# Kernel tuning notes

Hardware: AMD Instinct MI355X
Metric: run time of the kernel (lower is better)

## Reference

```python
import jax, jax.numpy as jnp
import numpy as np

NUM_CLASSES = 41
EPS = 1e-12


def nearest_resize(lab, h, w):
    # torch F.interpolate(mode='nearest'): src_idx = floor(dst_idx * in / out)
    Hl, Wl = lab.shape[1], lab.shape[2]
    ih = (jnp.arange(h) * Hl) // h
    iw = (jnp.arange(w) * Wl) // w
    return lab[:, ih][:, :, iw]


def segment_mean(feats, lab_small, base):
    # feats [b,c,h,w], lab_small [b,h,w] int, base [b,L,c] (values for absent labels)
    b, c, h, w = feats.shape
    L = NUM_CLASSES
    lab = lab_small.reshape(b, h * w)
    ids = (jnp.arange(b, dtype=lab.dtype)[:, None] * L + lab).reshape(-1)  # [b*h*w]
    x = feats.reshape(b, c, h * w).transpose(0, 2, 1).reshape(-1, c)       # [b*h*w, c]
    sums = jax.ops.segment_sum(x, ids, num_segments=b * L).reshape(b, L, c)
    cnts = jax.ops.segment_sum(jnp.ones((b * h * w,), feats.dtype), ids,
                               num_segments=b * L).reshape(b, L, 1)
    mean = sums / jnp.maximum(cnts, 1.0)
    return jnp.where(cnts > 0, mean, base)


def ra_gate(feats, lab_small, base, w1, w2):
    # RA.forward: segment-mean queue -> L2 normalize over class dim -> sum -> 1x1 convs -> sigmoid
    att = segment_mean(feats, lab_small, base)                      # [b,L,c]
    nrm = jnp.sqrt(jnp.sum(att * att, axis=1, keepdims=True))       # over classes (dim=1)
    att = att / jnp.maximum(nrm, EPS)
    s = jnp.sum(att, axis=1)                                        # [b,c]
    h1 = jax.nn.relu(jnp.einsum('bc,oc->bo', s, w1))                # conv1 1x1, no bias
    g = jax.nn.sigmoid(jnp.einsum('bo,co->bc', h1, w2))             # conv2 1x1, no bias
    return g[:, :, None, None]                                      # [b,c,1,1]


def conv3x3(x, w):
    return jax.lax.conv_general_dilated(
        x, w, window_strides=(1, 1), padding=((1, 1), (1, 1)),
        dimension_numbers=('NCHW', 'OIHW', 'NCHW'))


def setup_inputs() -> dict:
    key = jax.random.key(0)
    ks = jax.random.split(key, 10)
    B, C, H, W = 8, 128, 128, 128
    return {
        'r': jax.random.normal(ks[0], (B, C, H, W), jnp.float32),
        'd': jax.random.normal(ks[1], (B, C, H, W), jnp.float32),
        'label': jax.random.randint(ks[2], (B, 4 * H, 4 * W), 0, NUM_CLASSES, jnp.int32),
        'conv_w': jax.random.normal(ks[3], (C, 2 * C, 3, 3), jnp.float32) * 0.05,
        'f_w1': jax.random.normal(ks[4], (C // 16, C), jnp.float32) * 0.05,
        'f_w2': jax.random.normal(ks[5], (C, C // 16), jnp.float32) * 0.05,
        'd_w1': jax.random.normal(ks[6], (C // 16, C), jnp.float32) * 0.05,
        'd_w2': jax.random.normal(ks[7], (C, C // 16), jnp.float32) * 0.05,
        'seg_base_f': jax.random.normal(ks[8], (B, NUM_CLASSES, C), jnp.float32),
        'seg_base_d': jax.random.normal(ks[9], (B, NUM_CLASSES, C), jnp.float32),
    }


def reference(r, d, label, conv_w, f_w1, f_w2, d_w1, d_w2, seg_base_f, seg_base_d):
    b, c, h, w = r.shape
    add = r + d
    mul = r * jax.nn.sigmoid(d)
    fuse = conv3x3(jnp.concatenate([add, mul], axis=1), conv_w)
    lab_small = nearest_resize(label, h, w)
    d_ra = d * ra_gate(d, lab_small, seg_base_d, d_w1, d_w2)
    fuse_ra = fuse * ra_gate(fuse, lab_small, seg_base_f, f_w1, f_w2)
    return fuse_ra + d_ra
```

## Files before the change

kernel.cpp:

```cpp
#include <hip/hip_runtime.h>
#include <math.h>

typedef unsigned short u16;
typedef unsigned char u8;
typedef unsigned int u32;
typedef unsigned long long u64;
typedef __bf16 bf16x8 __attribute__((ext_vector_type(8)));
typedef float f32x4 __attribute__((ext_vector_type(4)));

#define NL 41
#define HW 16384

#define NHWC_OFF   0
#define WA_OFF     67108864
#define LAB8_OFF   67698688
#define SUMS_OFF   67829760
#define GATES_OFF  68165632
#define PD_OFF     68173824
#define PD_END     78921728ull

#define PSZ 5248

__device__ __forceinline__ u16 f2bf(float f) {
    u32 u = __builtin_bit_cast(u32, f);
    u = (u + 0x7FFFu + ((u >> 16) & 1u)) >> 16;
    return (u16)u;
}

__device__ __forceinline__ void glds16(const void* g, void* l) {
    __builtin_amdgcn_global_load_lds(
        (const __attribute__((address_space(1))) void*)g,
        (__attribute__((address_space(3))) void*)l, 16, 0, 0);
}

__global__ __launch_bounds__(256, 2)
void k_prep(const float* __restrict__ r, const float* __restrict__ d,
            const int* __restrict__ label, const float* __restrict__ w,
            u16* __restrict__ nhwc, u16* __restrict__ wa,
            u8* __restrict__ lab8, float* __restrict__ pd)
{
    __shared__ u16 s[64 * 256];
    __shared__ float binsd[NL * 256];
    __shared__ u8 s_lab[256];
    const int bid = (int)blockIdx.x;
    const int b = bid >> 6;
    const int px0 = (bid & 63) * 256;
    const int tid = (int)threadIdx.x;
    const int c = tid & 127;
    const int half = tid >> 7;

    if (bid < 144) {
        const int wi = bid * 4 + (tid >> 6);
        const int l = tid & 63;
        const int kt = wi >> 3, ct = wi & 7;
        const int chunk = kt / 9, tap = kt - chunk * 9;
        const int co = ct * 16 + (l & 15);
        const int cin0 = chunk * 32 + (l >> 4) * 8;
        u16 tmp[8];
#pragma unroll
        for (int j = 0; j < 8; ++j)
            tmp[j] = f2bf(w[((size_t)co * 256 + cin0 + j) * 9 + tap]);
        *(f32x4*)&wa[((size_t)wi * 64 + l) * 8] = *(f32x4*)tmp;
    }

    for (int i = tid; i < NL * 64; i += 256) ((f32x4*)binsd)[i] = f32x4{0,0,0,0};

    {
        int px = px0 + tid;
        int yy = px >> 7, xx = px & 127;
        int lab = label[(size_t)b * 512 * 512 + (yy * 4) * 512 + xx * 4];
        lab8[b * HW + px] = (u8)lab;
        s_lab[tid] = (u8)lab;
    }
    __syncthreads();

    for (int t = 0; t < 4; ++t) {
        const int pxb = px0 + t * 64 + half * 32;
        const float* rp = r + ((size_t)(b * 128 + c)) * HW + pxb;
        const float* dp = d + ((size_t)(b * 128 + c)) * HW + pxb;
        const u8* lp = &s_lab[t * 64 + half * 32];
        uint4 lw0 = *(const uint4*)lp;
        uint4 lw1 = *(const uint4*)(lp + 16);
        u32 lwords[8] = {lw0.x, lw0.y, lw0.z, lw0.w, lw1.x, lw1.y, lw1.z, lw1.w};
#pragma unroll
        for (int j = 0; j < 8; ++j) {
            float4 rv = *(const float4*)(rp + j * 4);
            float4 dv = *(const float4*)(dp + j * 4);
            float ra[4] = {rv.x, rv.y, rv.z, rv.w};
            float da[4] = {dv.x, dv.y, dv.z, dv.w};
#pragma unroll
            for (int i = 0; i < 4; ++i) {
                int pxl = half * 32 + j * 4 + i;
                s[pxl * 256 + c] = f2bf(ra[i] + da[i]);
                s[pxl * 256 + 128 + c] = f2bf(ra[i] / (1.f + __expf(-da[i])));
                int lab = (int)((lwords[j] >> (i * 8)) & 0xffu);
                binsd[lab * 256 + tid] += da[i];
            }
        }
        __syncthreads();
        const f32x4* sf = (const f32x4*)s;
        f32x4* dst = (f32x4*)nhwc + ((size_t)b * HW + px0 + t * 64) * 32;
#pragma unroll
        for (int k = 0; k < 8; ++k) {
            int fi = k * 256 + tid;
            dst[fi] = sf[fi];
        }
        __syncthreads();
    }
    float* pout = pd + (size_t)bid * PSZ;
    for (int i = tid; i < NL * 128; i += 256) {
        int lab = i >> 7, cc = i & 127;
        pout[i] = binsd[lab * 256 + cc] + binsd[lab * 256 + 128 + cc];
    }
}

__global__ __launch_bounds__(256, 2)
void k_conv(const u16* __restrict__ nhwc, const u16* __restrict__ wa,
            float* __restrict__ out)
{
    __shared__ u16 s_in[2 * 2080 * 8];
    const int tid = (int)threadIdx.x;
    const int bid = (int)blockIdx.x;
    const int b = bid & 7;
    const int y0 = (bid >> 3) * 2;
    const int l = tid & 63;
    const int wv = tid >> 6;
    const int wr = wv & 1;
    const int wc = wv >> 1;
    const int l15 = l & 15;
    const int l16 = l >> 4;

    {
        f32x4 zz = {0.f, 0.f, 0.f, 0.f};
        for (int i = tid; i < 4160; i += 256) ((f32x4*)s_in)[i] = zz;
    }

    int goff[9];
#pragma unroll
    for (int it = 0; it < 9; ++it) {
        int s = it * 256 + tid;
        int row = s / 520;
        int rem = s - row * 520;
        int xslot = rem >> 2;
        int ci8 = rem & 3;
        int gy = y0 - 1 + row;
        int gx = xslot - 1;
        bool valid = (s < 2080) && ((unsigned)gy < 128u) && ((unsigned)gx < 128u);
        goff[it] = valid ? (((gy << 7) | gx) * 256 + ci8 * 8) * 2 : -1;
    }

    f32x4 acc[4][8];
#pragma unroll
    for (int i = 0; i < 4; ++i)
#pragma unroll
        for (int j = 0; j < 8; ++j) {
            f32x4 zz = {0.f, 0.f, 0.f, 0.f};
            acc[i][j] = zz;
        }

    const char* src_b = (const char*)(nhwc + (size_t)b * HW * 256);
    const int lane_base = (tid & 192) * 16;
    const f32x4* wa4 = (const f32x4*)wa;

    __syncthreads();
#pragma unroll
    for (int it = 0; it < 9; ++it)
        if (goff[it] >= 0)
            glds16(src_b + goff[it], (char*)s_in + it * 4096 + lane_base);

#pragma unroll 1
    for (int chunk = 0; chunk < 8; ++chunk) {
        __syncthreads();

        f32x4 a0[4], a1[4];
        {
            int kt8 = chunk * 72;
#pragma unroll
            for (int i = 0; i < 4; ++i) a0[i] = wa4[(kt8 + wc * 4 + i) * 64 + l];
#pragma unroll
            for (int i = 0; i < 4; ++i) a1[i] = wa4[(kt8 + 8 + wc * 4 + i) * 64 + l];
        }
        if (chunk < 7) {
            char* dstb = (char*)s_in + ((chunk + 1) & 1) * 33280 + lane_base;
#pragma unroll
            for (int it = 0; it < 9; ++it)
                if (goff[it] >= 0)
                    glds16(src_b + goff[it] + (chunk + 1) * 64, dstb + it * 4096);
        }

        const char* bufp = (const char*)s_in + (chunk & 1) * 33280;
#pragma unroll
        for (int tap = 0; tap < 9; ++tap) {
            f32x4 aC[4];
#pragma unroll
            for (int i = 0; i < 4; ++i) aC[i] = a0[i];
#pragma unroll
            for (int i = 0; i < 4; ++i) a0[i] = a1[i];
            if (tap + 2 < 9) {
                int kt8 = chunk * 72 + (tap + 2) * 8;
#pragma unroll
                for (int i = 0; i < 4; ++i)
                    a1[i] = wa4[(kt8 + wc * 4 + i) * 64 + l];
            }
            const int rowi = wr + tap / 3;
            const int dxo = tap % 3;
            f32x4 bf[8];
#pragma unroll
            for (int p = 0; p < 8; ++p) {
                int e = (rowi * 130 + p * 16 + l15 + dxo) * 64 + l16 * 16;
                bf[p] = *(const f32x4*)(bufp + e);
            }
#pragma unroll
            for (int ct = 0; ct < 4; ++ct) {
                bf16x8 av = __builtin_bit_cast(bf16x8, aC[ct]);
#pragma unroll
                for (int p = 0; p < 8; ++p)
                    acc[ct][p] = __builtin_amdgcn_mfma_f32_16x16x32_bf16(
                        av, __builtin_bit_cast(bf16x8, bf[p]), acc[ct][p], 0, 0, 0);
            }
        }
    }

    const int y = y0 + wr;
    float* outb = out + (size_t)b * 128 * HW + (size_t)y * 128;
#pragma unroll
    for (int ct = 0; ct < 4; ++ct)
#pragma unroll
        for (int p = 0; p < 8; ++p) {
            int x = p * 16 + l15;
#pragma unroll
            for (int rr = 0; rr < 4; ++rr) {
                int co = wc * 64 + ct * 16 + l16 * 4 + rr;
                outb[(size_t)co * HW + x] = acc[ct][p][rr];
            }
        }
}

__global__ __launch_bounds__(256, 3)
void k_seg2(const float* __restrict__ fuse, const float* __restrict__ pd,
            const u8* __restrict__ lab8, float* __restrict__ sums_f,
            float* __restrict__ sums_d)
{
    __shared__ float bins[NL][256];
    const int bid = (int)blockIdx.x;
    const int tid = (int)threadIdx.x;

    if (bid >= 1024) {
        const int idx = bid - 1024;
        if (tid < 128) {
            const int b = idx / 41, lab = idx - b * 41;
            const float* q = pd + (size_t)b * 64 * PSZ + lab * 128 + tid;
            float sv = 0.f;
#pragma unroll 8
            for (int k = 0; k < 64; ++k) sv += q[(size_t)k * PSZ];
            sums_d[(size_t)idx * 128 + tid] = sv;
        }
        return;
    }

    const int c = bid & 127;
    const int b = bid >> 7;

    for (int i = tid; i < NL * 256; i += 256) ((float*)bins)[i] = 0.f;
    __syncthreads();

    const float* src = fuse + ((size_t)(b * 128 + c)) * HW;
    const u8* lp = lab8 + b * HW;

#pragma unroll 4
    for (int k = 0; k < 16; ++k) {
        int i = k * 256 + tid;
        float4 v = ((const float4*)src)[i];
        uchar4 lv = ((const uchar4*)lp)[i];
        bins[lv.x][tid] += v.x;
        bins[lv.y][tid] += v.y;
        bins[lv.z][tid] += v.z;
        bins[lv.w][tid] += v.w;
    }
    __syncthreads();

    for (int stride = 128; stride >= 1; stride >>= 1) {
        for (int idx = tid; idx < NL * stride; idx += 256) {
            int l = idx / stride;
            int cc = idx - l * stride;
            bins[l][cc] += bins[l][cc + stride];
        }
        __syncthreads();
    }
    if (tid < NL)
        sums_f[(size_t)(b * NL + tid) * 128 + c] = bins[tid][0];
}

__global__ __launch_bounds__(128)
void k_gates(const float* __restrict__ sums, const u8* __restrict__ lab8,
             const float* __restrict__ base_f, const float* __restrict__ base_d,
             const float* __restrict__ f_w1, const float* __restrict__ f_w2,
             const float* __restrict__ d_w1, const float* __restrict__ d_w2,
             float* __restrict__ gates)
{
    __shared__ float sv[128];
    __shared__ float h1[8];
    __shared__ int hist[NL];
    const int b = (int)blockIdx.x >> 1;
    const int feat = (int)blockIdx.x & 1;
    const int c = (int)threadIdx.x;

    if (c < NL) hist[c] = 0;
    __syncthreads();
    {
        const uchar4* lp = (const uchar4*)(lab8 + (size_t)b * HW);
        for (int k = 0; k < 32; ++k) {
            uchar4 lv = lp[c + k * 128];
            atomicAdd(&hist[lv.x], 1);
            atomicAdd(&hist[lv.y], 1);
            atomicAdd(&hist[lv.z], 1);
            atomicAdd(&hist[lv.w], 1);
        }
    }
    __syncthreads();

    const float* base = feat ? base_d : base_f;
    const float* sf = sums + (size_t)feat * 8 * NL * 128;
    float suma = 0.f, sumsq = 0.f;
    for (int lc = 0; lc < NL; ++lc) {
        float s = sf[(size_t)(b * NL + lc) * 128 + c];
        int cnt = hist[lc];
        float att = (cnt > 0) ? (s / (float)cnt) : base[(b * NL + lc) * 128 + c];
        suma += att;
        sumsq += att * att;
    }
    sv[c] = suma / fmaxf(sqrtf(sumsq), 1e-12f);
    __syncthreads();

    const float* w1 = feat ? d_w1 : f_w1;
    const float* w2 = feat ? d_w2 : f_w2;
    if (c < 8) {
        float h = 0.f;
        for (int k = 0; k < 128; ++k) h += w1[c * 128 + k] * sv[k];
        h1[c] = fmaxf(h, 0.f);
    }
    __syncthreads();

    float gv = 0.f;
#pragma unroll
    for (int o = 0; o < 8; ++o) gv += w2[c * 8 + o] * h1[o];
    gates[feat * 1024 + b * 128 + c] = 1.f / (1.f + expf(-gv));
}

__global__ __launch_bounds__(256)
void k_final(const float* __restrict__ d, const float* __restrict__ gates,
             float* out)
{
    const size_t base = (size_t)blockIdx.x * 256 + threadIdx.x;
#pragma unroll
    for (int it = 0; it < 8; ++it) {
        size_t t4 = base + (size_t)it * (2048 * 256);
        size_t basei = t4 * 4;
        int bc = (int)(basei >> 14);
        float gf = gates[bc];
        float gd = gates[1024 + bc];
        float4 f = *(const float4*)(out + basei);
        float4 dv = *(const float4*)(d + basei);
        float4 o;
        o.x = f.x * gf + dv.x * gd;
        o.y = f.y * gf + dv.y * gd;
        o.z = f.z * gf + dv.z * gd;
        o.w = f.w * gf + dv.w * gd;
        *(float4*)(out + basei) = o;
    }
}

__global__ __launch_bounds__(128)
void k_red(const float* __restrict__ p, float* __restrict__ sout)
{
    const int bid = (int)blockIdx.x;
    const int b = bid / 41, lab = bid - b * 41;
    const int c = (int)threadIdx.x;
    const float* q = p + (size_t)b * 64 * PSZ + lab * 128 + c;
    float s = 0.f;
#pragma unroll 8
    for (int k = 0; k < 64; ++k) s += q[(size_t)k * PSZ];
    sout[(size_t)bid * 128 + c] = s;
}

extern "C" void kernel_launch(void* const* d_in, const int* in_sizes, int n_in,
                              void* d_out, int out_size, void* d_ws, size_t ws_size,
                              hipStream_t stream)
{
    (void)in_sizes; (void)n_in; (void)out_size;
    const float* r      = (const float*)d_in[0];
    const float* d      = (const float*)d_in[1];
    const int*   label  = (const int*)d_in[2];
    const float* conv_w = (const float*)d_in[3];
    const float* f_w1   = (const float*)d_in[4];
    const float* f_w2   = (const float*)d_in[5];
    const float* d_w1   = (const float*)d_in[6];
    const float* d_w2   = (const float*)d_in[7];
    const float* base_f = (const float*)d_in[8];
    const float* base_d = (const float*)d_in[9];
    float* out = (float*)d_out;

    char* ws = (char*)d_ws;
    u16* nhwc     = (u16*)(ws + NHWC_OFF);
    u16* wa       = (u16*)(ws + WA_OFF);
    u8*  lab8     = (u8*)(ws + LAB8_OFF);
    float* sums   = (float*)(ws + SUMS_OFF);
    float* sums_f = sums;
    float* sums_d = sums + 8 * NL * 128;
    float* gates  = (float*)(ws + GATES_OFF);

    const bool big = ws_size >= PD_END;
    float* pd = big ? (float*)(ws + PD_OFF) : (float*)d_out;

    hipLaunchKernelGGL(k_prep, dim3(512), dim3(256), 0, stream, r, d, label,
                       conv_w, nhwc, wa, lab8, pd);
    if (!big)
        hipLaunchKernelGGL(k_red, dim3(328), dim3(128), 0, stream, pd, sums_d);
    hipLaunchKernelGGL(k_conv, dim3(512), dim3(256), 0, stream, nhwc, wa, out);
    hipLaunchKernelGGL(k_seg2, dim3(big ? 1352 : 1024), dim3(256), 0, stream,
                       out, pd, lab8, sums_f, sums_d);
    hipLaunchKernelGGL(k_gates, dim3(16), dim3(128), 0, stream, sums, lab8,
                       base_f, base_d, f_w1, f_w2, d_w1, d_w2, gates);
    hipLaunchKernelGGL(k_final, dim3(2048), dim3(256), 0, stream, d, gates, out);
}
```

Measured before the change: 368.5 us.

## Split conv tiles along width and move label histogram into prep kernel

The conv kernel now tiles 2 rows by 64 columns instead of 2 full rows. This halves LDS use and accumulator registers, doubles the grid to 1024 blocks and raises the launch-bounds occupancy hint to 3. The cost is extra halo reloads at the column split. Per-batch label counts are now built inside k_prep with shared atomics and merged into a global histogram, which is zeroed by a memset first. This takes the serial 16-block histogram loop out of k_gates, at the price of an extra memset and global atomics.

```diff
diff --git a/kernel.cpp b/kernel.cpp
--- a/kernel.cpp
+++ b/kernel.cpp
@@ -16,8 +16,9 @@
 #define LAB8_OFF   67698688
 #define SUMS_OFF   67829760
 #define GATES_OFF  68165632
-#define PD_OFF     68173824
-#define PD_END     78921728ull
+#define GH_OFF     68173824
+#define PD_OFF     68177920
+#define PD_END     78925824ull
 
 #define PSZ 5248
 
@@ -37,11 +38,13 @@
 void k_prep(const float* __restrict__ r, const float* __restrict__ d,
             const int* __restrict__ label, const float* __restrict__ w,
             u16* __restrict__ nhwc, u16* __restrict__ wa,
-            u8* __restrict__ lab8, float* __restrict__ pd)
+            u8* __restrict__ lab8, float* __restrict__ pd,
+            int* __restrict__ ghist)
 {
     __shared__ u16 s[64 * 256];
     __shared__ float binsd[NL * 256];
     __shared__ u8 s_lab[256];
+    __shared__ int hist[NL];
     const int bid = (int)blockIdx.x;
     const int b = bid >> 6;
     const int px0 = (bid & 63) * 256;
@@ -63,7 +66,9 @@
         *(f32x4*)&wa[((size_t)wi * 64 + l) * 8] = *(f32x4*)tmp;
     }
 
+    if (tid < NL) hist[tid] = 0;
     for (int i = tid; i < NL * 64; i += 256) ((f32x4*)binsd)[i] = f32x4{0,0,0,0};
+    __syncthreads();
 
     {
         int px = px0 + tid;
@@ -71,6 +76,7 @@
         int lab = label[(size_t)b * 512 * 512 + (yy * 4) * 512 + xx * 4];
         lab8[b * HW + px] = (u8)lab;
         s_lab[tid] = (u8)lab;
+        atomicAdd(&hist[lab], 1);
     }
     __syncthreads();
 
@@ -112,17 +118,19 @@
         int lab = i >> 7, cc = i & 127;
         pout[i] = binsd[lab * 256 + cc] + binsd[lab * 256 + 128 + cc];
     }
-}
-
-__global__ __launch_bounds__(256, 2)
+    if (tid < NL && hist[tid] > 0) atomicAdd(&ghist[b * NL + tid], hist[tid]);
+}
+
+__global__ __launch_bounds__(256, 3)
 void k_conv(const u16* __restrict__ nhwc, const u16* __restrict__ wa,
             float* __restrict__ out)
 {
-    __shared__ u16 s_in[2 * 2080 * 8];
+    __shared__ u16 s_in[2 * 1056 * 8];
     const int tid = (int)threadIdx.x;
     const int bid = (int)blockIdx.x;
     const int b = bid & 7;
-    const int y0 = (bid >> 3) * 2;
+    const int y0 = ((bid >> 3) & 63) * 2;
+    const int x0 = (bid >> 9) * 64;
     const int l = tid & 63;
     const int wv = tid >> 6;
     const int wr = wv & 1;
@@ -132,28 +140,28 @@
 
     {
         f32x4 zz = {0.f, 0.f, 0.f, 0.f};
-        for (int i = tid; i < 4160; i += 256) ((f32x4*)s_in)[i] = zz;
-    }
-
-    int goff[9];
-#pragma unroll
-    for (int it = 0; it < 9; ++it) {
+        for (int i = tid; i < 2112; i += 256) ((f32x4*)s_in)[i] = zz;
+    }
+
+    int goff[5];
+#pragma unroll
+    for (int it = 0; it < 5; ++it) {
         int s = it * 256 + tid;
-        int row = s / 520;
-        int rem = s - row * 520;
+        int row = s / 264;
+        int rem = s - row * 264;
         int xslot = rem >> 2;
         int ci8 = rem & 3;
         int gy = y0 - 1 + row;
-        int gx = xslot - 1;
-        bool valid = (s < 2080) && ((unsigned)gy < 128u) && ((unsigned)gx < 128u);
+        int gx = x0 - 1 + xslot;
+        bool valid = (s < 1056) && ((unsigned)gy < 128u) && ((unsigned)gx < 128u);
         goff[it] = valid ? (((gy << 7) | gx) * 256 + ci8 * 8) * 2 : -1;
     }
 
-    f32x4 acc[4][8];
+    f32x4 acc[4][4];
 #pragma unroll
     for (int i = 0; i < 4; ++i)
 #pragma unroll
-        for (int j = 0; j < 8; ++j) {
+        for (int j = 0; j < 4; ++j) {
             f32x4 zz = {0.f, 0.f, 0.f, 0.f};
             acc[i][j] = zz;
         }
@@ -164,7 +172,7 @@
 
     __syncthreads();
 #pragma unroll
-    for (int it = 0; it < 9; ++it)
+    for (int it = 0; it < 5; ++it)
         if (goff[it] >= 0)
             glds16(src_b + goff[it], (char*)s_in + it * 4096 + lane_base);
 
@@ -181,14 +189,14 @@
             for (int i = 0; i < 4; ++i) a1[i] = wa4[(kt8 + 8 + wc * 4 + i) * 64 + l];
         }
         if (chunk < 7) {
-            char* dstb = (char*)s_in + ((chunk + 1) & 1) * 33280 + lane_base;
-#pragma unroll
-            for (int it = 0; it < 9; ++it)
+            char* dstb = (char*)s_in + ((chunk + 1) & 1) * 16896 + lane_base;
+#pragma unroll
+            for (int it = 0; it < 5; ++it)
                 if (goff[it] >= 0)
                     glds16(src_b + goff[it] + (chunk + 1) * 64, dstb + it * 4096);
         }
 
-        const char* bufp = (const char*)s_in + (chunk & 1) * 33280;
+        const char* bufp = (const char*)s_in + (chunk & 1) * 16896;
 #pragma unroll
         for (int tap = 0; tap < 9; ++tap) {
             f32x4 aC[4];
@@ -204,17 +212,17 @@
             }
             const int rowi = wr + tap / 3;
             const int dxo = tap % 3;
-            f32x4 bf[8];
-#pragma unroll
-            for (int p = 0; p < 8; ++p) {
-                int e = (rowi * 130 + p * 16 + l15 + dxo) * 64 + l16 * 16;
+            f32x4 bf[4];
+#pragma unroll
+            for (int p = 0; p < 4; ++p) {
+                int e = (rowi * 66 + p * 16 + l15 + dxo) * 64 + l16 * 16;
                 bf[p] = *(const f32x4*)(bufp + e);
             }
 #pragma unroll
             for (int ct = 0; ct < 4; ++ct) {
                 bf16x8 av = __builtin_bit_cast(bf16x8, aC[ct]);
 #pragma unroll
-                for (int p = 0; p < 8; ++p)
+                for (int p = 0; p < 4; ++p)
                     acc[ct][p] = __builtin_amdgcn_mfma_f32_16x16x32_bf16(
                         av, __builtin_bit_cast(bf16x8, bf[p]), acc[ct][p], 0, 0, 0);
             }
@@ -226,8 +234,8 @@
 #pragma unroll
     for (int ct = 0; ct < 4; ++ct)
 #pragma unroll
-        for (int p = 0; p < 8; ++p) {
-            int x = p * 16 + l15;
+        for (int p = 0; p < 4; ++p) {
+            int x = x0 + p * 16 + l15;
 #pragma unroll
             for (int rr = 0; rr < 4; ++rr) {
                 int co = wc * 64 + ct * 16 + l16 * 4 + rr;
@@ -292,7 +300,7 @@
 }
 
 __global__ __launch_bounds__(128)
-void k_gates(const float* __restrict__ sums, const u8* __restrict__ lab8,
+void k_gates(const float* __restrict__ sums, const int* __restrict__ ghist,
              const float* __restrict__ base_f, const float* __restrict__ base_d,
              const float* __restrict__ f_w1, const float* __restrict__ f_w2,
              const float* __restrict__ d_w1, const float* __restrict__ d_w2,
@@ -300,31 +308,16 @@
 {
     __shared__ float sv[128];
     __shared__ float h1[8];
-    __shared__ int hist[NL];
     const int b = (int)blockIdx.x >> 1;
     const int feat = (int)blockIdx.x & 1;
     const int c = (int)threadIdx.x;
-
-    if (c < NL) hist[c] = 0;
-    __syncthreads();
-    {
-        const uchar4* lp = (const uchar4*)(lab8 + (size_t)b * HW);
-        for (int k = 0; k < 32; ++k) {
-            uchar4 lv = lp[c + k * 128];
-            atomicAdd(&hist[lv.x], 1);
-            atomicAdd(&hist[lv.y], 1);
-            atomicAdd(&hist[lv.z], 1);
-            atomicAdd(&hist[lv.w], 1);
-        }
-    }
-    __syncthreads();
 
     const float* base = feat ? base_d : base_f;
     const float* sf = sums + (size_t)feat * 8 * NL * 128;
     float suma = 0.f, sumsq = 0.f;
     for (int lc = 0; lc < NL; ++lc) {
         float s = sf[(size_t)(b * NL + lc) * 128 + c];
-        int cnt = hist[lc];
+        int cnt = ghist[b * NL + lc];
         float att = (cnt > 0) ? (s / (float)cnt) : base[(b * NL + lc) * 128 + c];
         suma += att;
         sumsq += att * att;
@@ -408,18 +401,20 @@
     float* sums_f = sums;
     float* sums_d = sums + 8 * NL * 128;
     float* gates  = (float*)(ws + GATES_OFF);
+    int* ghist    = (int*)(ws + GH_OFF);
 
     const bool big = ws_size >= PD_END;
     float* pd = big ? (float*)(ws + PD_OFF) : (float*)d_out;
 
+    hipMemsetAsync(ghist, 0, 8 * NL * sizeof(int), stream);
     hipLaunchKernelGGL(k_prep, dim3(512), dim3(256), 0, stream, r, d, label,
-                       conv_w, nhwc, wa, lab8, pd);
+                       conv_w, nhwc, wa, lab8, pd, ghist);
     if (!big)
         hipLaunchKernelGGL(k_red, dim3(328), dim3(128), 0, stream, pd, sums_d);
-    hipLaunchKernelGGL(k_conv, dim3(512), dim3(256), 0, stream, nhwc, wa, out);
+    hipLaunchKernelGGL(k_conv, dim3(1024), dim3(256), 0, stream, nhwc, wa, out);
     hipLaunchKernelGGL(k_seg2, dim3(big ? 1352 : 1024), dim3(256), 0, stream,
                        out, pd, lab8, sums_f, sums_d);
-    hipLaunchKernelGGL(k_gates, dim3(16), dim3(128), 0, stream, sums, lab8,
+    hipLaunchKernelGGL(k_gates, dim3(16), dim3(128), 0, stream, sums, ghist,
                        base_f, base_d, f_w1, f_w2, d_w1, d_w2, gates);
     hipLaunchKernelGGL(k_final, dim3(2048), dim3(256), 0, stream, d, gates, out);
 }
```

Result: slower. 397.5 us (+7.9%).
